# Optimization experiments

Measured on AMD Instinct MI355X. Metric: run time of the kernel, lower is better.

The kernel has to match this reference:

```python
import jax, jax.numpy as jnp
import numpy as np

H = 128
K = 20
N = 100000
B = 65536
TIME_SCALE = 1.0
NEG = -1e9


def setup_inputs() -> dict:
    key = jax.random.key(0)
    ks = jax.random.split(key, 16)
    s = 0.05
    return {
        "edge_index": jax.random.randint(ks[0], (2, B), 0, N),
        "edge_timestamp": jax.random.randint(ks[1], (B,), 0, 1000000),
        "hist_neighbors": jax.random.randint(ks[2], (N, K), 0, N),
        "hist_times": jax.random.randint(ks[3], (N, K), 0, 1000000),
        "hist_signs": jax.random.randint(ks[4], (N, K), 0, 2),
        "node_emb": jax.random.normal(ks[5], (N, H), jnp.float32) * s,
        "sign_emb": jax.random.normal(ks[6], (2, H), jnp.float32) * s,
        "tp_w1": jax.random.normal(ks[7], (H,), jnp.float32) * s,   # Linear(1,H) weight (flattened)
        "tp_b1": jax.random.normal(ks[8], (H,), jnp.float32) * s,
        "tp_w2": jax.random.normal(ks[9], (H, H), jnp.float32) * s,  # stored [in,out]
        "tp_b2": jax.random.normal(ks[10], (H,), jnp.float32) * s,
        "em_w1": jax.random.normal(ks[11], (4 * H, H), jnp.float32) * s,
        "em_b1": jax.random.normal(ks[12], (H,), jnp.float32) * s,
        "em_w2": jax.random.normal(ks[13], (H, 1), jnp.float32) * s,
        "em_b2": jax.random.normal(ks[14], (1,), jnp.float32) * s,
    }


def _encode(node_ids, query_times, hist_neighbors, hist_times, hist_signs,
            node_emb, sign_emb, tp_w1, tp_b1, tp_w2, tp_b2):
    # node_ids, query_times: [B]
    neigh = hist_neighbors[node_ids]   # [B,K]
    times = hist_times[node_ids]       # [B,K]
    signs = hist_signs[node_ids]       # [B,K]
    valid = (neigh != -1) & (times < query_times[:, None])
    neigh_c = jnp.where(neigh == -1, 0, neigh)
    neigh_e = node_emb[neigh_c]        # [B,K,H]
    sign_e = sign_emb[signs]           # [B,K,H]
    delta = (query_times[:, None].astype(jnp.float32) - times.astype(jnp.float32)) / TIME_SCALE
    h = jax.nn.relu(delta[..., None] * tp_w1 + tp_b1)           # [B,K,H]
    time_e = jnp.einsum('bkh,hd->bkd', h, tp_w2) + tp_b2        # [B,K,H]
    keys = neigh_e + sign_e + time_e
    query = node_emb[node_ids][:, None]                          # [B,1,H]
    scores = jnp.sum(query * keys, axis=-1) / jnp.sqrt(jnp.float32(H))
    scores = jnp.where(valid, scores, NEG)
    attn = jax.nn.softmax(scores, axis=1)                        # [B,K]
    return jnp.einsum('bk,bkh->bh', attn, keys)                  # [B,H]


def reference(edge_index, edge_timestamp, hist_neighbors, hist_times, hist_signs,
              node_emb, sign_emb, tp_w1, tp_b1, tp_w2, tp_b2,
              em_w1, em_b1, em_w2, em_b2):
    u, v = edge_index[0], edge_index[1]
    zu = _encode(u, edge_timestamp, hist_neighbors, hist_times, hist_signs,
                 node_emb, sign_emb, tp_w1, tp_b1, tp_w2, tp_b2)
    zv = _encode(v, edge_timestamp, hist_neighbors, hist_times, hist_signs,
                 node_emb, sign_emb, tp_w1, tp_b1, tp_w2, tp_b2)
    feat = jnp.concatenate([zu, zv, jnp.abs(zu - zv), zu * zv], axis=1)  # [B,4H]
    hid = jax.nn.relu(feat @ em_w1 + em_b1)
    logits = (hid @ em_w2 + em_b2).squeeze(-1)                           # [B]
    return logits
```

## Files before the change

kernel.cpp:

```cpp
#include <hip/hip_runtime.h>
#include <hip/hip_bf16.h>
#include <math.h>

#define H 128
#define K 20
#define EPB 16

#define WS_TBL    0
#define WS_THM    65792
#define WS_CNT    66176
#define WSB_HI    67072
#define WSB_LO    99840

typedef __attribute__((ext_vector_type(8))) short short8;
typedef __attribute__((ext_vector_type(4))) float f32x4;

template<int CTRL, int RMASK>
__device__ __forceinline__ float dpp_add(float x) {
  int y = __builtin_amdgcn_update_dpp(0, __float_as_int(x), CTRL, RMASK, 0xf, true);
  return x + __int_as_float(y);
}
__device__ __forceinline__ float wave_sum63(float x) {
  x = dpp_add<0xB1,  0xf>(x);
  x = dpp_add<0x4E,  0xf>(x);
  x = dpp_add<0x141, 0xf>(x);
  x = dpp_add<0x140, 0xf>(x);
  x = dpp_add<0x142, 0xa>(x);
  x = dpp_add<0x143, 0xc>(x);
  return x;
}
__device__ __forceinline__ float bcast63(float x) {
  return __int_as_float(__builtin_amdgcn_readlane(__float_as_int(x), 63));
}

template<int CTRL>
__device__ __forceinline__ float dpp_mov(float x) {
  return __int_as_float(
      __builtin_amdgcn_update_dpp(0, __float_as_int(x), CTRL, 0xf, 0xf, true));
}
template<int L>
__device__ __forceinline__ float rdlane(float x) {
  return __int_as_float(__builtin_amdgcn_readlane(__float_as_int(x), L));
}
template<int CTRL>
__device__ __forceinline__ float merge2(float z0, float z1, bool beta) {
  float keep = beta ? z1 : z0;
  float sel  = beta ? z0 : z1;
  return keep + dpp_mov<CTRL>(sel);
}
__device__ __forceinline__ float red2(float z0, float z1, bool b0) {
  float r = merge2<0xB1>(z0, z1, b0);
  r += dpp_mov<0x4E>(r);
  r += dpp_mov<0x124>(r);
  r += dpp_mov<0x128>(r);
  r += __shfl_xor(r, 16);
  r += __shfl_xor(r, 32);
  return r;
}

__device__ __forceinline__ unsigned short bfbits(float x) {
  __hip_bfloat16 h = __float2bfloat16(x);
  unsigned short u; __builtin_memcpy(&u, &h, 2); return u;
}
__device__ __forceinline__ float bf2f(unsigned short u) {
  return __uint_as_float(((unsigned)u) << 16);
}

__global__ __launch_bounds__(128) void aux_kernel(
    const float* __restrict__ w1v, const float* __restrict__ b1v,
    const float* __restrict__ w2, const float* __restrict__ b2,
    const float* __restrict__ em_w1, float* __restrict__ ws)
{
  int blk = blockIdx.x;
  int tid = threadIdx.x;
  if (blk < 257) {
    __shared__ float th[H];
    __shared__ int grp[H];
    __shared__ int sidx[2 * H];
    __shared__ int Msh;
    float w = w1v[tid], b = b1v[tid];
    int g = (w > 0.f) ? 0 : ((w < 0.f) ? 1 : 2);
    float t = (g == 2) ? 0.f : (-b / w);
    th[tid] = t; grp[tid] = g;
    if (tid == 0) Msh = 0;
    __syncthreads();
    if (g != 2) {
      int r = 0;
      for (int i = 0; i < H; i++)
        if (grp[i] != 2 && (th[i] < t || (th[i] == t && i < tid))) r++;
      sidx[r] = (tid << 1) | (g == 0 ? 1 : 0);
      atomicAdd(&Msh, 1);
      if (blk == 0) ws[WS_THM + r] = t;
    }
    __syncthreads();
    int M = Msh;
    if (blk == 0 && tid == 0) ((int*)(ws + WS_CNT))[0] = M;
    int r = blk;
    if (r > M) return;
    int d = tid;
    float accW = 0.f, accB = b2[d];
    for (int i = 0; i < H; i++)
      if (grp[i] == 2 && b1v[i] > 0.f) accB += b1v[i] * w2[i * H + d];
    #pragma unroll 4
    for (int i = 0; i < M; i++) {
      int ent = sidx[i];
      int h = ent >> 1;
      int isP = ent & 1;
      int take = (i < r) ? isP : (1 - isP);
      if (take) {
        float wv = w2[h * H + d];
        accW += w1v[h] * wv;
        accB += b1v[h] * wv;
      }
    }
    ws[WS_TBL + r * 256 + 2 * d + 0] = accW;
    ws[WS_TBL + r * 256 + 2 * d + 1] = accB;
  } else {
    int idx = (blk - 257) * 128 + tid;
    int j  = idx & 7;
    int l  = (idx >> 3) & 63;
    int kc = (idx >> 9) & 15;
    int c  = idx >> 13;
    int k = kc * 32 + ((l >> 4) * 8) + j;
    int n = c * 16 + (l & 15);
    float x = em_w1[k * H + n];
    unsigned short hb = bfbits(x);
    unsigned short lb = bfbits(x - bf2f(hb));
    ((unsigned short*)(ws + WSB_HI))[idx] = hb;
    ((unsigned short*)(ws + WSB_LO))[idx] = lb;
  }
}

template<int NB>
__device__ __forceinline__ void run_sides(
    int sbase, int b0, int B, int lane,
    const int* __restrict__ edge_index, const int* __restrict__ edge_ts,
    const int* __restrict__ hist_nb, const int* __restrict__ hist_tm,
    const int* __restrict__ hist_sg,
    const float* __restrict__ node_emb, const float* __restrict__ ws,
    float th0, float th1, float th2, float th3,
    float2 se0, float2 se1, float* __restrict__ zbuf)
{
  const float S = 0.088388347648318447f;
  const bool b0sel = (lane & 1) != 0;
  int eBase = sbase >> 1;
  int eN = b0 + eBase;
  int nU = edge_index[eN];
  int nV = edge_index[B + eN];
  int t_n = edge_ts[eN];
  float2 qU_n = *(const float2*)(node_emb + (size_t)nU * H + 2 * lane);
  float2 qV_n = *(const float2*)(node_emb + (size_t)nV * H + 2 * lane);
  int pkU_n = 0, tmU_n = 0, pkV_n = 0, tmV_n = 0;
  if (lane < K) {
    pkU_n = (hist_nb[nU * K + lane] << 1) | hist_sg[nU * K + lane];
    tmU_n = hist_tm[nU * K + lane];
    pkV_n = (hist_nb[nV * K + lane] << 1) | hist_sg[nV * K + lane];
    tmV_n = hist_tm[nV * K + lane];
  }

  #pragma unroll 1
  for (int p = 0; p < 4; p++) {
    int e = eBase + p;
    int tC = t_n;
    float2 qU = qU_n, qV = qV_n;
    int pkU = pkU_n, tmU = tmU_n, pkV = pkV_n, tmV = tmV_n;
    if (p < 3) {
      int e2 = b0 + e + 1;
      int nU2 = edge_index[e2];
      int nV2 = edge_index[B + e2];
      t_n = edge_ts[e2];
      qU_n = *(const float2*)(node_emb + (size_t)nU2 * H + 2 * lane);
      qV_n = *(const float2*)(node_emb + (size_t)nV2 * H + 2 * lane);
      if (lane < K) {
        pkU_n = (hist_nb[nU2 * K + lane] << 1) | hist_sg[nU2 * K + lane];
        tmU_n = hist_tm[nU2 * K + lane];
        pkV_n = (hist_nb[nV2 * K + lane] << 1) | hist_sg[nV2 * K + lane];
        tmV_n = hist_tm[nV2 * K + lane];
      }
    }

    unsigned long long mU0 = __ballot((lane < K) && (tmU < tC) && (pkU >= 0));
    unsigned long long mV0 = __ballot((lane < K) && (tmV < tC) && (pkV >= 0));
    bool fU = (mU0 == 0), fV = (mV0 == 0);
    unsigned long long mU = fU ? 0xFFFFFull : mU0;
    unsigned long long mV = fV ? 0xFFFFFull : mV0;
    float qUx = qU.x * S, qUy = qU.y * S;
    float qVx = qV.x * S, qVy = qV.y * S;

    float mxU = -3.0e38f, ssU = 0.f, zU0 = 0.f, zU1 = 0.f;
    float mxV = -3.0e38f, ssV = 0.f, zV0 = 0.f, zV1 = 0.f;

    #define RANK4(d) (__popcll(__ballot(th0 < (d))) + __popcll(__ballot(th1 < (d))) \
                      + (NB == 4 ? (__popcll(__ballot(th2 < (d))) + __popcll(__ballot(th3 < (d)))) : 0))

    while (mU | mV) {
      bool vUa = mU != 0; int kUa = vUa ? __ffsll((long long)mU) - 1 : 0; mU &= mU - 1;
      bool vUb = mU != 0; int kUb = vUb ? __ffsll((long long)mU) - 1 : 0; mU &= mU - 1;
      bool vUc = mU != 0; int kUc = vUc ? __ffsll((long long)mU) - 1 : 0; mU &= mU - 1;
      bool vUd = mU != 0; int kUd = vUd ? __ffsll((long long)mU) - 1 : 0; mU &= mU - 1;
      bool vVa = mV != 0; int kVa = vVa ? __ffsll((long long)mV) - 1 : 0; mV &= mV - 1;
      bool vVb = mV != 0; int kVb = vVb ? __ffsll((long long)mV) - 1 : 0; mV &= mV - 1;
      bool vVc = mV != 0; int kVc = vVc ? __ffsll((long long)mV) - 1 : 0; mV &= mV - 1;
      bool vVd = mV != 0; int kVd = vVd ? __ffsll((long long)mV) - 1 : 0; mV &= mV - 1;

      int tmUa = __builtin_amdgcn_readlane(tmU, kUa), pkUa = __builtin_amdgcn_readlane(pkU, kUa);
      int tmUb = __builtin_amdgcn_readlane(tmU, kUb), pkUb = __builtin_amdgcn_readlane(pkU, kUb);
      int tmUc = __builtin_amdgcn_readlane(tmU, kUc), pkUc = __builtin_amdgcn_readlane(pkU, kUc);
      int tmUd = __builtin_amdgcn_readlane(tmU, kUd), pkUd = __builtin_amdgcn_readlane(pkU, kUd);
      int tmVa = __builtin_amdgcn_readlane(tmV, kVa), pkVa = __builtin_amdgcn_readlane(pkV, kVa);
      int tmVb = __builtin_amdgcn_readlane(tmV, kVb), pkVb = __builtin_amdgcn_readlane(pkV, kVb);
      int tmVc = __builtin_amdgcn_readlane(tmV, kVc), pkVc = __builtin_amdgcn_readlane(pkV, kVc);
      int tmVd = __builtin_amdgcn_readlane(tmV, kVd), pkVd = __builtin_amdgcn_readlane(pkV, kVd);

      float dUa = (float)(tC - tmUa), dUb = (float)(tC - tmUb);
      float dUc = (float)(tC - tmUc), dUd = (float)(tC - tmUd);
      float dVa = (float)(tC - tmVa), dVb = (float)(tC - tmVb);
      float dVc = (float)(tC - tmVc), dVd = (float)(tC - tmVd);

      int rUa = RANK4(dUa), rUb = RANK4(dUb), rUc = RANK4(dUc), rUd = RANK4(dUd);
      int rVa = RANK4(dVa), rVb = RANK4(dVb), rVc = RANK4(dVc), rVd = RANK4(dVd);

      const float4 tbUa = *(const float4*)(ws + WS_TBL + rUa * 256 + 4 * lane);
      const float4 tbUb = *(const float4*)(ws + WS_TBL + rUb * 256 + 4 * lane);
      const float4 tbUc = *(const float4*)(ws + WS_TBL + rUc * 256 + 4 * lane);
      const float4 tbUd = *(const float4*)(ws + WS_TBL + rUd * 256 + 4 * lane);
      const float4 tbVa = *(const float4*)(ws + WS_TBL + rVa * 256 + 4 * lane);
      const float4 tbVb = *(const float4*)(ws + WS_TBL + rVb * 256 + 4 * lane);
      const float4 tbVc = *(const float4*)(ws + WS_TBL + rVc * 256 + 4 * lane);
      const float4 tbVd = *(const float4*)(ws + WS_TBL + rVd * 256 + 4 * lane);
      float2 neUa = *(const float2*)(node_emb + (size_t)(pkUa >> 1) * H + 2 * lane);
      float2 neUb = *(const float2*)(node_emb + (size_t)(pkUb >> 1) * H + 2 * lane);
      float2 neUc = *(const float2*)(node_emb + (size_t)(pkUc >> 1) * H + 2 * lane);
      float2 neUd = *(const float2*)(node_emb + (size_t)(pkUd >> 1) * H + 2 * lane);
      float2 neVa = *(const float2*)(node_emb + (size_t)(pkVa >> 1) * H + 2 * lane);
      float2 neVb = *(const float2*)(node_emb + (size_t)(pkVb >> 1) * H + 2 * lane);
      float2 neVc = *(const float2*)(node_emb + (size_t)(pkVc >> 1) * H + 2 * lane);
      float2 neVd = *(const float2*)(node_emb + (size_t)(pkVd >> 1) * H + 2 * lane);
      __builtin_amdgcn_sched_barrier(0);

      float kU0a = neUa.x + ((pkUa & 1) ? se1.x : se0.x) + dUa * tbUa.x + tbUa.y;
      float kU1a = neUa.y + ((pkUa & 1) ? se1.y : se0.y) + dUa * tbUa.z + tbUa.w;
      float kU0b = neUb.x + ((pkUb & 1) ? se1.x : se0.x) + dUb * tbUb.x + tbUb.y;
      float kU1b = neUb.y + ((pkUb & 1) ? se1.y : se0.y) + dUb * tbUb.z + tbUb.w;
      float kU0c = neUc.x + ((pkUc & 1) ? se1.x : se0.x) + dUc * tbUc.x + tbUc.y;
      float kU1c = neUc.y + ((pkUc & 1) ? se1.y : se0.y) + dUc * tbUc.z + tbUc.w;
      float kU0d = neUd.x + ((pkUd & 1) ? se1.x : se0.x) + dUd * tbUd.x + tbUd.y;
      float kU1d = neUd.y + ((pkUd & 1) ? se1.y : se0.y) + dUd * tbUd.z + tbUd.w;
      float kV0a = neVa.x + ((pkVa & 1) ? se1.x : se0.x) + dVa * tbVa.x + tbVa.y;
      float kV1a = neVa.y + ((pkVa & 1) ? se1.y : se0.y) + dVa * tbVa.z + tbVa.w;
      float kV0b = neVb.x + ((pkVb & 1) ? se1.x : se0.x) + dVb * tbVb.x + tbVb.y;
      float kV1b = neVb.y + ((pkVb & 1) ? se1.y : se0.y) + dVb * tbVb.z + tbVb.w;
      float kV0c = neVc.x + ((pkVc & 1) ? se1.x : se0.x) + dVc * tbVc.x + tbVc.y;
      float kV1c = neVc.y + ((pkVc & 1) ? se1.y : se0.y) + dVc * tbVc.z + tbVc.w;
      float kV0d = neVd.x + ((pkVd & 1) ? se1.x : se0.x) + dVd * tbVd.x + tbVd.y;
      float kV1d = neVd.y + ((pkVd & 1) ? se1.y : se0.y) + dVd * tbVd.z + tbVd.w;

      float p0 = qUx * kU0a + qUy * kU1a;
      float p1 = qUx * kU0b + qUy * kU1b;
      float p2 = qUx * kU0c + qUy * kU1c;
      float p3 = qUx * kU0d + qUy * kU1d;
      float p4 = qVx * kV0a + qVy * kV1a;
      float p5 = qVx * kV0b + qVy * kV1b;
      float p6 = qVx * kV0c + qVy * kV1c;
      float p7 = qVx * kV0d + qVy * kV1d;
      float cU01 = red2(p0, p1, b0sel);
      float cU23 = red2(p2, p3, b0sel);
      float cV01 = red2(p4, p5, b0sel);
      float cV23 = red2(p6, p7, b0sel);

      float sUa = vUa ? (fU ? -1e9f : rdlane<0>(cU01)) : -3.0e38f;
      float sUb = vUb ? (fU ? -1e9f : rdlane<1>(cU01)) : -3.0e38f;
      float sUc = vUc ? (fU ? -1e9f : rdlane<0>(cU23)) : -3.0e38f;
      float sUd = vUd ? (fU ? -1e9f : rdlane<1>(cU23)) : -3.0e38f;
      float sVa = vVa ? (fV ? -1e9f : rdlane<0>(cV01)) : -3.0e38f;
      float sVb = vVb ? (fV ? -1e9f : rdlane<1>(cV01)) : -3.0e38f;
      float sVc = vVc ? (fV ? -1e9f : rdlane<0>(cV23)) : -3.0e38f;
      float sVd = vVd ? (fV ? -1e9f : rdlane<1>(cV23)) : -3.0e38f;

      float mnU = fmaxf(fmaxf(mxU, fmaxf(sUa, sUb)), fmaxf(sUc, sUd));
      float alU = __expf(mxU - mnU);
      float wUa = __expf(sUa - mnU), wUb = __expf(sUb - mnU);
      float wUc = __expf(sUc - mnU), wUd = __expf(sUd - mnU);
      ssU = ssU * alU + ((wUa + wUb) + (wUc + wUd));
      zU0 = zU0 * alU + ((wUa * kU0a + wUb * kU0b) + (wUc * kU0c + wUd * kU0d));
      zU1 = zU1 * alU + ((wUa * kU1a + wUb * kU1b) + (wUc * kU1c + wUd * kU1d));
      mxU = mnU;

      float mnV = fmaxf(fmaxf(mxV, fmaxf(sVa, sVb)), fmaxf(sVc, sVd));
      float alV = __expf(mxV - mnV);
      float wVa = __expf(sVa - mnV), wVb = __expf(sVb - mnV);
      float wVc = __expf(sVc - mnV), wVd = __expf(sVd - mnV);
      ssV = ssV * alV + ((wVa + wVb) + (wVc + wVd));
      zV0 = zV0 * alV + ((wVa * kV0a + wVb * kV0b) + (wVc * kV0c + wVd * kV0d));
      zV1 = zV1 * alV + ((wVa * kV1a + wVb * kV1b) + (wVc * kV1c + wVd * kV1d));
      mxV = mnV;
    }
    #undef RANK4

    float invU = 1.f / ssU; zU0 *= invU; zU1 *= invU;
    float invV = 1.f / ssV; zV0 *= invV; zV1 *= invV;

    int sw = (e & 7) << 1;
    int ccU = lane ^ sw;
    int ccV = (64 + lane) ^ sw;
    *(float2*)&zbuf[(e << 8) + (ccU << 1)] = make_float2(zU0, zU1);
    *(float2*)&zbuf[(e << 8) + (ccV << 1)] = make_float2(zV0, zV1);
  }
}

__global__ __launch_bounds__(256, 4) void tgat_main_kernel(
    const int* __restrict__ edge_index, const int* __restrict__ edge_ts,
    const int* __restrict__ hist_nb, const int* __restrict__ hist_tm,
    const int* __restrict__ hist_sg,
    const float* __restrict__ node_emb, const float* __restrict__ sign_emb,
    const float* __restrict__ em_b1,
    const float* __restrict__ em_w2, const float* __restrict__ em_b2,
    const float* __restrict__ ws, float* __restrict__ out, int B)
{
  __shared__ __align__(16) float zbuf[EPB * 256];

  int tid = threadIdx.x;
  int lane = tid & 63;
  int wv = __builtin_amdgcn_readfirstlane(tid >> 6);
  int b0 = blockIdx.x * EPB;

  int M = ((const int*)(ws + WS_CNT))[0];
  float th0 = (lane       < M) ? ws[WS_THM + lane      ] : 3.0e38f;
  float th1 = (lane + 64  < M) ? ws[WS_THM + lane + 64 ] : 3.0e38f;
  float2 se0 = *(const float2*)(sign_emb + 2 * lane);
  float2 se1 = *(const float2*)(sign_emb + H + 2 * lane);

  int sbase = wv * 8;
  if (M <= 128) {
    run_sides<2>(sbase, b0, B, lane, edge_index, edge_ts, hist_nb, hist_tm,
                 hist_sg, node_emb, ws, th0, th1, 3.0e38f, 3.0e38f,
                 se0, se1, zbuf);
  } else {
    float th2 = (lane + 128 < M) ? ws[WS_THM + lane + 128] : 3.0e38f;
    float th3 = (lane + 192 < M) ? ws[WS_THM + lane + 192] : 3.0e38f;
    run_sides<4>(sbase, b0, B, lane, edge_index, edge_ts, hist_nb, hist_tm,
                 hist_sg, node_emb, ws, th0, th1, th2, th3,
                 se0, se1, zbuf);
  }
  __syncthreads();

  const unsigned short* whi = (const unsigned short*)(ws + WSB_HI);
  const unsigned short* wlo = (const unsigned short*)(ws + WSB_LO);
  int c0 = 2 * wv;
  int m_ = lane & 15;
  int qd = lane >> 4;
  int sw = (m_ & 7) << 1;
  const float* zrow = zbuf + (m_ << 8);
  f32x4 acc0 = {0.f, 0.f, 0.f, 0.f};
  f32x4 acc1 = {0.f, 0.f, 0.f, 0.f};
  #pragma unroll
  for (int kc = 0; kc < 16; kc++) {
    const int reg = kc >> 2;
    int cb = (kc & 3) * 16 + qd * 4;
    float av[8];
    if (reg == 0) {
      float4 A0 = *(const float4*)(zrow + (((cb    ) ^ sw) << 1));
      float4 A1 = *(const float4*)(zrow + (((cb + 2) ^ sw) << 1));
      av[0]=A0.x; av[1]=A0.y; av[2]=A0.z; av[3]=A0.w;
      av[4]=A1.x; av[5]=A1.y; av[6]=A1.z; av[7]=A1.w;
    } else if (reg == 1) {
      float4 A0 = *(const float4*)(zrow + (((cb + 64) ^ sw) << 1));
      float4 A1 = *(const float4*)(zrow + (((cb + 66) ^ sw) << 1));
      av[0]=A0.x; av[1]=A0.y; av[2]=A0.z; av[3]=A0.w;
      av[4]=A1.x; av[5]=A1.y; av[6]=A1.z; av[7]=A1.w;
    } else {
      float4 U0 = *(const float4*)(zrow + (((cb    ) ^ sw) << 1));
      float4 U1 = *(const float4*)(zrow + (((cb + 2) ^ sw) << 1));
      float4 V0 = *(const float4*)(zrow + (((cb + 64) ^ sw) << 1));
      float4 V1 = *(const float4*)(zrow + (((cb + 66) ^ sw) << 1));
      float uu[8] = {U0.x,U0.y,U0.z,U0.w,U1.x,U1.y,U1.z,U1.w};
      float vvv[8] = {V0.x,V0.y,V0.z,V0.w,V1.x,V1.y,V1.z,V1.w};
      if (reg == 2) {
        #pragma unroll
        for (int j = 0; j < 8; j++) av[j] = fabsf(uu[j] - vvv[j]);
      } else {
        #pragma unroll
        for (int j = 0; j < 8; j++) av[j] = uu[j] * vvv[j];
      }
    }
    union { short8 v; unsigned u[4]; } ahi, alo;
    #pragma unroll
    for (int j = 0; j < 4; j++) {
      unsigned b0u = __float_as_uint(av[2 * j]);
      unsigned b1u = __float_as_uint(av[2 * j + 1]);
      ahi.u[j] = __builtin_amdgcn_perm(b1u, b0u, 0x07060302u);
      float l0 = av[2 * j]     - __uint_as_float(b0u & 0xFFFF0000u);
      float l1 = av[2 * j + 1] - __uint_as_float(b1u & 0xFFFF0000u);
      __hip_bfloat162 lp = __float22bfloat162_rn(make_float2(l0, l1));
      __builtin_memcpy(&alo.u[j], &lp, 4);
    }
    int f0 = (((c0    ) * 16 + kc) * 64 + lane) * 8;
    int f1 = (((c0 + 1) * 16 + kc) * 64 + lane) * 8;
    short8 bh0 = *(const short8*)(whi + f0);
    short8 bl0 = *(const short8*)(wlo + f0);
    short8 bh1 = *(const short8*)(whi + f1);
    short8 bl1 = *(const short8*)(wlo + f1);
    acc0 = __builtin_amdgcn_mfma_f32_16x16x32_bf16(ahi.v, bh0, acc0, 0, 0, 0);
    acc0 = __builtin_amdgcn_mfma_f32_16x16x32_bf16(ahi.v, bl0, acc0, 0, 0, 0);
    acc0 = __builtin_amdgcn_mfma_f32_16x16x32_bf16(alo.v, bh0, acc0, 0, 0, 0);
    acc1 = __builtin_amdgcn_mfma_f32_16x16x32_bf16(ahi.v, bh1, acc1, 0, 0, 0);
    acc1 = __builtin_amdgcn_mfma_f32_16x16x32_bf16(ahi.v, bl1, acc1, 0, 0, 0);
    acc1 = __builtin_amdgcn_mfma_f32_16x16x32_bf16(alo.v, bh1, acc1, 0, 0, 0);
  }
  __syncthreads();

  float* hp = zbuf;
  float eb0 = em_b1[c0 * 16 + m_];
  float eb1 = em_b1[(c0 + 1) * 16 + m_];
  #pragma unroll
  for (int r = 0; r < 4; r++) {
    int edge = qd * 4 + r;
    hp[edge * 132 + c0 * 16 + m_]       = fmaxf(acc0[r] + eb0, 0.f);
    hp[edge * 132 + (c0 + 1) * 16 + m_] = fmaxf(acc1[r] + eb1, 0.f);
  }
  __syncthreads();

  float2 w2v = *(const float2*)(em_w2 + 2 * lane);
  float bias2 = em_b2[0];
  #pragma unroll
  for (int i = 0; i < 4; i++) {
    int e = wv * 4 + i;
    int b = b0 + e;
    float2 hv = *(const float2*)(hp + e * 132 + 2 * lane);
    float p = wave_sum63(hv.x * w2v.x + hv.y * w2v.y);
    float ps = bcast63(p);
    if (lane == 0 && b < B) out[b] = ps + bias2;
  }
}

extern "C" void kernel_launch(void* const* d_in, const int* in_sizes, int n_in,
                              void* d_out, int out_size, void* d_ws, size_t ws_size,
                              hipStream_t stream)
{
  (void)n_in; (void)out_size; (void)ws_size;
  const int* edge_index = (const int*)d_in[0];
  const int* edge_ts    = (const int*)d_in[1];
  const int* hist_nb    = (const int*)d_in[2];
  const int* hist_tm    = (const int*)d_in[3];
  const int* hist_sg    = (const int*)d_in[4];
  const float* node_emb = (const float*)d_in[5];
  const float* sign_emb = (const float*)d_in[6];
  const float* tp_w1    = (const float*)d_in[7];
  const float* tp_b1    = (const float*)d_in[8];
  const float* tp_w2    = (const float*)d_in[9];
  const float* tp_b2    = (const float*)d_in[10];
  const float* em_w1    = (const float*)d_in[11];
  const float* em_b1    = (const float*)d_in[12];
  const float* em_w2    = (const float*)d_in[13];
  const float* em_b2    = (const float*)d_in[14];
  float* out = (float*)d_out;
  float* ws  = (float*)d_ws;
  int B = in_sizes[1];

  hipLaunchKernelGGL(aux_kernel, dim3(769), dim3(128), 0, stream,
                     tp_w1, tp_b1, tp_w2, tp_b2, em_w1, ws);
  int grid = (B + EPB - 1) / EPB;
  hipLaunchKernelGGL(tgat_main_kernel, dim3(grid), dim3(256), 0, stream,
                     edge_index, edge_ts, hist_nb, hist_tm, hist_sg,
                     node_emb, sign_emb, em_b1, em_w2, em_b2, ws, out, B);
}
```

Measured before the change: 355.2 us.

## Use 8 waves per block with 2 edges per wave and one MFMA column tile each

The block grows from 256 to 512 threads while still handling 16 edges. Each wave now encodes 2 edges instead of 4 and computes one 16-wide output column tile of the MLP instead of two. The aim is to shorten the serial per-wave encode loop and expose more parallelism for hiding gather latency. In exchange, launch_bounds(512,4) squeezes the register budget per thread, which risks spilling or lower occupancy, and each block now carries more barrier and sync overhead.

```diff
diff --git a/kernel.cpp b/kernel.cpp
--- a/kernel.cpp
+++ b/kernel.cpp
@@ -5,6 +5,7 @@
 #define H 128
 #define K 20
 #define EPB 16
+#define EPW 2
 
 #define WS_TBL    0
 #define WS_THM    65792
@@ -133,7 +134,7 @@
 
 template<int NB>
 __device__ __forceinline__ void run_sides(
-    int sbase, int b0, int B, int lane,
+    int eBase, int b0, int B, int lane,
     const int* __restrict__ edge_index, const int* __restrict__ edge_ts,
     const int* __restrict__ hist_nb, const int* __restrict__ hist_tm,
     const int* __restrict__ hist_sg,
@@ -143,7 +144,6 @@
 {
   const float S = 0.088388347648318447f;
   const bool b0sel = (lane & 1) != 0;
-  int eBase = sbase >> 1;
   int eN = b0 + eBase;
   int nU = edge_index[eN];
   int nV = edge_index[B + eN];
@@ -159,12 +159,12 @@
   }
 
   #pragma unroll 1
-  for (int p = 0; p < 4; p++) {
+  for (int p = 0; p < EPW; p++) {
     int e = eBase + p;
     int tC = t_n;
     float2 qU = qU_n, qV = qV_n;
     int pkU = pkU_n, tmU = tmU_n, pkV = pkV_n, tmV = tmV_n;
-    if (p < 3) {
+    if (p < EPW - 1) {
       int e2 = b0 + e + 1;
       int nU2 = edge_index[e2];
       int nV2 = edge_index[B + e2];
@@ -308,7 +308,7 @@
   }
 }
 
-__global__ __launch_bounds__(256, 4) void tgat_main_kernel(
+__global__ __launch_bounds__(512, 4) void tgat_main_kernel(
     const int* __restrict__ edge_index, const int* __restrict__ edge_ts,
     const int* __restrict__ hist_nb, const int* __restrict__ hist_tm,
     const int* __restrict__ hist_sg,
@@ -330,15 +330,15 @@
   float2 se0 = *(const float2*)(sign_emb + 2 * lane);
   float2 se1 = *(const float2*)(sign_emb + H + 2 * lane);
 
-  int sbase = wv * 8;
+  int eBase = wv * EPW;
   if (M <= 128) {
-    run_sides<2>(sbase, b0, B, lane, edge_index, edge_ts, hist_nb, hist_tm,
+    run_sides<2>(eBase, b0, B, lane, edge_index, edge_ts, hist_nb, hist_tm,
                  hist_sg, node_emb, ws, th0, th1, 3.0e38f, 3.0e38f,
                  se0, se1, zbuf);
   } else {
     float th2 = (lane + 128 < M) ? ws[WS_THM + lane + 128] : 3.0e38f;
     float th3 = (lane + 192 < M) ? ws[WS_THM + lane + 192] : 3.0e38f;
-    run_sides<4>(sbase, b0, B, lane, edge_index, edge_ts, hist_nb, hist_tm,
+    run_sides<4>(eBase, b0, B, lane, edge_index, edge_ts, hist_nb, hist_tm,
                  hist_sg, node_emb, ws, th0, th1, th2, th3,
                  se0, se1, zbuf);
   }
@@ -346,13 +346,12 @@
 
   const unsigned short* whi = (const unsigned short*)(ws + WSB_HI);
   const unsigned short* wlo = (const unsigned short*)(ws + WSB_LO);
-  int c0 = 2 * wv;
+  int c0 = wv;
   int m_ = lane & 15;
   int qd = lane >> 4;
   int sw = (m_ & 7) << 1;
   const float* zrow = zbuf + (m_ << 8);
   f32x4 acc0 = {0.f, 0.f, 0.f, 0.f};
-  f32x4 acc1 = {0.f, 0.f, 0.f, 0.f};
   #pragma unroll
   for (int kc = 0; kc < 16; kc++) {
     const int reg = kc >> 2;
@@ -394,37 +393,29 @@
       __hip_bfloat162 lp = __float22bfloat162_rn(make_float2(l0, l1));
       __builtin_memcpy(&alo.u[j], &lp, 4);
     }
-    int f0 = (((c0    ) * 16 + kc) * 64 + lane) * 8;
-    int f1 = (((c0 + 1) * 16 + kc) * 64 + lane) * 8;
+    int f0 = ((c0 * 16 + kc) * 64 + lane) * 8;
     short8 bh0 = *(const short8*)(whi + f0);
     short8 bl0 = *(const short8*)(wlo + f0);
-    short8 bh1 = *(const short8*)(whi + f1);
-    short8 bl1 = *(const short8*)(wlo + f1);
     acc0 = __builtin_amdgcn_mfma_f32_16x16x32_bf16(ahi.v, bh0, acc0, 0, 0, 0);
     acc0 = __builtin_amdgcn_mfma_f32_16x16x32_bf16(ahi.v, bl0, acc0, 0, 0, 0);
     acc0 = __builtin_amdgcn_mfma_f32_16x16x32_bf16(alo.v, bh0, acc0, 0, 0, 0);
-    acc1 = __builtin_amdgcn_mfma_f32_16x16x32_bf16(ahi.v, bh1, acc1, 0, 0, 0);
-    acc1 = __builtin_amdgcn_mfma_f32_16x16x32_bf16(ahi.v, bl1, acc1, 0, 0, 0);
-    acc1 = __builtin_amdgcn_mfma_f32_16x16x32_bf16(alo.v, bh1, acc1, 0, 0, 0);
   }
   __syncthreads();
 
   float* hp = zbuf;
   float eb0 = em_b1[c0 * 16 + m_];
-  float eb1 = em_b1[(c0 + 1) * 16 + m_];
   #pragma unroll
   for (int r = 0; r < 4; r++) {
     int edge = qd * 4 + r;
-    hp[edge * 132 + c0 * 16 + m_]       = fmaxf(acc0[r] + eb0, 0.f);
-    hp[edge * 132 + (c0 + 1) * 16 + m_] = fmaxf(acc1[r] + eb1, 0.f);
+    hp[edge * 132 + c0 * 16 + m_] = fmaxf(acc0[r] + eb0, 0.f);
   }
   __syncthreads();
 
   float2 w2v = *(const float2*)(em_w2 + 2 * lane);
   float bias2 = em_b2[0];
   #pragma unroll
-  for (int i = 0; i < 4; i++) {
-    int e = wv * 4 + i;
+  for (int i = 0; i < EPW; i++) {
+    int e = wv * EPW + i;
     int b = b0 + e;
     float2 hv = *(const float2*)(hp + e * 132 + 2 * lane);
     float p = wave_sum63(hv.x * w2v.x + hv.y * w2v.y);
@@ -460,7 +451,7 @@
   hipLaunchKernelGGL(aux_kernel, dim3(769), dim3(128), 0, stream,
                      tp_w1, tp_b1, tp_w2, tp_b2, em_w1, ws);
   int grid = (B + EPB - 1) / EPB;
-  hipLaunchKernelGGL(tgat_main_kernel, dim3(grid), dim3(256), 0, stream,
+  hipLaunchKernelGGL(tgat_main_kernel, dim3(grid), dim3(512), 0, stream,
                      edge_index, edge_ts, hist_nb, hist_tm, hist_sg,
                      node_emb, sign_emb, em_b1, em_w2, em_b2, ws, out, B);
 }
```

Result: slower. 365.5 us (+2.9%).
